# Kernel tuning notes

Measured on AMD Instinct MI355X. Metric: run time of the kernel, lower is better.

Reference implementation:

```python
import jax, jax.numpy as jnp
import numpy as np

N, D, K = 262144, 128, 1024

def setup_inputs() -> dict:
    key = jax.random.key(0)
    kx, km = jax.random.split(key)
    X = jax.random.normal(kx, (N, D), dtype=jnp.float32)
    means = jax.random.normal(km, (K, D), dtype=jnp.float32)
    return {"X": X, "means": means}

def reference(X, means):
    X2 = jnp.sum(X * X, axis=1, keepdims=True)            # [n, 1]
    m2 = jnp.sum(means * means, axis=1)[None, :]          # [1, k]
    dists = X2 - 2.0 * jnp.einsum('nd,kd->nk', X, means) + m2
    assignments = jnp.argmin(dists, axis=1)               # [n]
    approx_X = means[assignments]                         # gather [n, d]
    loss = jnp.sum(jnp.square(X - approx_X))
    return loss
```

## Files before the change

kernel.cpp:

```cpp
#include <hip/hip_runtime.h>
#include <hip/hip_fp8.h>

typedef int v8i __attribute__((ext_vector_type(8)));
typedef float f32x4 __attribute__((ext_vector_type(4)));

#define N_TOTAL 262144
#define D 128
#define K_TOTAL 1024
#define BN 128
#define NBLK (N_TOTAL / BN)
#define TILEB 8192
#define NT 16

__device__ __forceinline__ unsigned umx(unsigned a, unsigned b) {
  return a > b ? a : b;
}

__global__ void prep_means(const float* __restrict__ means,
                           unsigned char* __restrict__ mbf8,
                           float* __restrict__ nm2) {
  int k = blockIdx.x, t = threadIdx.x;
  int ts = k >> 6, c64 = k & 63;
  int cgc = c64 >> 4, c = c64 & 15;
  unsigned char* tb = mbf8 + ts * TILEB + cgc * 2048;
  float v0 = means[k * D + 2 * t];
  float v1 = means[k * D + 2 * t + 1];
  int d0 = 2 * t;
  int kq = d0 >> 5, rem0 = d0 & 31;
  int pk = __builtin_amdgcn_cvt_pk_fp8_f32(v0, v1, 0, false);
  *(unsigned short*)(tb + (kq * 16 + c) * 32 + rem0) = (unsigned short)(pk & 0xFFFF);
  float s = v0 * v0 + v1 * v1;
#pragma unroll
  for (int m = 32; m; m >>= 1) s += __shfl_down(s, m, 64);
  if (t == 0) nm2[k] = -0.5f * s;
}

union BOp {
  uint4 q[2];
  v8i v;
};

__global__ __launch_bounds__(256) void kmeans_main(
    const float* __restrict__ X, const unsigned char* __restrict__ mbf8,
    const float* __restrict__ nm2, float* __restrict__ partials) {
  __shared__ float m2s[K_TOTAL];
  __shared__ float x2s[BN];
  __shared__ float wsum[4];

  const int t = threadIdx.x;
  const int l = t & 63;
  const int w = t >> 6;
  const int lr = l & 15;
  const int kq = l >> 4;
  const long nbase = (long)blockIdx.x * BN;

  v8i af[2];
  float psq[2];
#pragma unroll
  for (int g = 0; g < 2; ++g) {
    const float* xr = X + (nbase + w * 32 + g * 16 + lr) * D + kq * 32;
    v8i av;
    float sq = 0.f;
#pragma unroll
    for (int j = 0; j < 8; ++j) {
      float4 v = *(const float4*)(xr + j * 4);
      sq = fmaf(v.x, v.x, sq);
      sq = fmaf(v.y, v.y, sq);
      sq = fmaf(v.z, v.z, sq);
      sq = fmaf(v.w, v.w, sq);
      int lo = __builtin_amdgcn_cvt_pk_fp8_f32(v.x, v.y, 0, false);
      av[j] = __builtin_amdgcn_cvt_pk_fp8_f32(v.z, v.w, lo, true);
    }
    af[g] = av;
    psq[g] = sq;
  }
#pragma unroll
  for (int g = 0; g < 2; ++g) {
    float s2 = psq[g];
    s2 += __shfl_xor(s2, 16, 64);
    s2 += __shfl_xor(s2, 32, 64);
    if (kq == 0) x2s[w * 32 + g * 16 + lr] = s2;
  }

  {
    float4 v = ((const float4*)nm2)[t];
    *(float4*)(m2s + t * 4) = v;
  }

  float bs[8];
#pragma unroll
  for (int e = 0; e < 8; ++e) bs[e] = -3.402823466e38f;

  __syncthreads();

  const char* bbase = (const char*)mbf8 + l * 32;
  for (int ts = 0; ts < NT; ++ts) {
    const char* tp = bbase + ts * TILEB;
    const float* mp = m2s + ts * 64 + lr;
#pragma unroll
    for (int cgc = 0; cgc < 4; ++cgc) {
      const char* p = tp + cgc * 2048;
      BOp bu;
      bu.q[0] = *(const uint4*)(p);
      bu.q[1] = *(const uint4*)(p + 16);
      float m2v = mp[cgc * 16];
      f32x4 ci = {m2v, m2v, m2v, m2v};
#pragma unroll
      for (int g = 0; g < 2; ++g) {
        f32x4 acc = __builtin_amdgcn_mfma_scale_f32_16x16x128_f8f6f4(
            af[g], bu.v, ci, 0, 0, 0, 127, 0, 127);
#pragma unroll
        for (int e = 0; e < 4; ++e) bs[g * 4 + e] = fmaxf(bs[g * 4 + e], acc[e]);
      }
    }
  }

  float lsum = 0.f;
#pragma unroll
  for (int e = 0; e < 8; ++e) {
    float m = bs[e];
#pragma unroll
    for (int s = 1; s < 16; s <<= 1) {
      float o = __shfl_xor(m, s, 64);
      m = fmaxf(m, o);
    }
    if (lr == 0) {
      int rowc = (e >> 2) * 16 + kq * 4 + (e & 3);
      lsum += x2s[w * 32 + rowc] - 2.0f * m;
    }
  }
#pragma unroll
  for (int s = 32; s; s >>= 1) lsum += __shfl_down(lsum, s, 64);
  if (l == 0) wsum[w] = lsum;
  __syncthreads();
  if (t == 0) partials[blockIdx.x] = wsum[0] + wsum[1] + wsum[2] + wsum[3];
}

__global__ void reduce_loss(const float* __restrict__ partials,
                            float* __restrict__ out) {
  __shared__ double ws[4];
  int t = threadIdx.x;
  double s = 0.0;
  for (int i = t; i < NBLK; i += 256) s += (double)partials[i];
#pragma unroll
  for (int m = 32; m; m >>= 1) s += __shfl_down(s, m, 64);
  if ((t & 63) == 0) ws[t >> 6] = s;
  __syncthreads();
  if (t == 0) out[0] = (float)(ws[0] + ws[1] + ws[2] + ws[3]);
}

extern "C" void kernel_launch(void* const* d_in, const int* in_sizes, int n_in,
                              void* d_out, int out_size, void* d_ws,
                              size_t ws_size, hipStream_t stream) {
  const float* X = (const float*)d_in[0];
  const float* means = (const float*)d_in[1];
  float* out = (float*)d_out;
  char* ws = (char*)d_ws;
  unsigned char* mbf8 = (unsigned char*)ws;
  float* nm2 = (float*)(ws + 131072);
  float* partials = (float*)(ws + 131072 + 4096);

  prep_means<<<K_TOTAL, 64, 0, stream>>>(means, mbf8, nm2);
  kmeans_main<<<NBLK, 256, 0, stream>>>(X, mbf8, nm2, partials);
  reduce_loss<<<1, 256, 0, stream>>>(partials, out);
}
```

Baseline: 74.67 us.

## Split X fp8 conversion into separate prep kernel feeding MFMA-ready layout

Adds a prep_x kernel that converts X to fp8 in the MFMA operand layout and computes row norms into global memory. The main kernel then loads packed fp8 operands directly, with no LDS staging and no __syncthreads before the matmul loop, and reads the centroid norms from global memory. This costs an extra kernel launch plus a write and reread of a 32MB fp8 buffer. A fallback path keeps the old fused kernel when the workspace is too small.

```diff
diff --git a/kernel.cpp b/kernel.cpp
--- a/kernel.cpp
+++ b/kernel.cpp
@@ -12,8 +12,8 @@
 #define TILEB 8192
 #define NT 16
 
-__device__ __forceinline__ unsigned umx(unsigned a, unsigned b) {
-  return a > b ? a : b;
+__device__ __forceinline__ unsigned f2fp8_em(float x) {
+  return (unsigned)__hip_fp8_e4m3(x).__x;
 }
 
 __global__ void prep_means(const float* __restrict__ means,
@@ -28,11 +28,45 @@
   int d0 = 2 * t;
   int kq = d0 >> 5, rem0 = d0 & 31;
   int pk = __builtin_amdgcn_cvt_pk_fp8_f32(v0, v1, 0, false);
-  *(unsigned short*)(tb + (kq * 16 + c) * 32 + rem0) = (unsigned short)(pk & 0xFFFF);
+  *(unsigned short*)(tb + (kq * 16 + c) * 32 + rem0) =
+      (unsigned short)(pk & 0xFFFF);
   float s = v0 * v0 + v1 * v1;
 #pragma unroll
   for (int m = 32; m; m >>= 1) s += __shfl_down(s, m, 64);
   if (t == 0) nm2[k] = -0.5f * s;
+}
+
+__global__ __launch_bounds__(256) void prep_x(const float* __restrict__ X,
+                                              unsigned char* __restrict__ xp,
+                                              float* __restrict__ x2g) {
+  const int t = threadIdx.x;
+  const long row = (long)blockIdx.x * BN + (t >> 1);
+  const int h = t & 1;
+  const float* xr = X + row * D + h * 64;
+  unsigned cw[16];
+  float sq = 0.f;
+#pragma unroll
+  for (int j = 0; j < 16; ++j) {
+    float4 v = *(const float4*)(xr + j * 4);
+    sq = fmaf(v.x, v.x, sq);
+    sq = fmaf(v.y, v.y, sq);
+    sq = fmaf(v.z, v.z, sq);
+    sq = fmaf(v.w, v.w, sq);
+    int lo = __builtin_amdgcn_cvt_pk_fp8_f32(v.x, v.y, 0, false);
+    cw[j] = (unsigned)__builtin_amdgcn_cvt_pk_fp8_f32(v.z, v.w, lo, true);
+  }
+  unsigned char* gb = xp + (row >> 4) * 2048 + (int)(row & 15) * 32;
+#pragma unroll
+  for (int q = 0; q < 2; ++q) {
+    uint4 a, b;
+    a.x = cw[q * 8 + 0]; a.y = cw[q * 8 + 1]; a.z = cw[q * 8 + 2]; a.w = cw[q * 8 + 3];
+    b.x = cw[q * 8 + 4]; b.y = cw[q * 8 + 5]; b.z = cw[q * 8 + 6]; b.w = cw[q * 8 + 7];
+    unsigned char* d0 = gb + (h * 2 + q) * 512;
+    *(uint4*)d0 = a;
+    *(uint4*)(d0 + 16) = b;
+  }
+  float s2 = sq + __shfl_xor(sq, 1, 64);
+  if (h == 0) x2g[row] = s2;
 }
 
 union BOp {
@@ -41,10 +75,9 @@
 };
 
 __global__ __launch_bounds__(256) void kmeans_main(
-    const float* __restrict__ X, const unsigned char* __restrict__ mbf8,
-    const float* __restrict__ nm2, float* __restrict__ partials) {
-  __shared__ float m2s[K_TOTAL];
-  __shared__ float x2s[BN];
+    const unsigned char* __restrict__ xp, const unsigned char* __restrict__ mbf8,
+    const float* __restrict__ nm2, const float* __restrict__ x2g,
+    float* __restrict__ partials) {
   __shared__ float wsum[4];
 
   const int t = threadIdx.x;
@@ -55,6 +88,78 @@
   const long nbase = (long)blockIdx.x * BN;
 
   v8i af[2];
+  {
+    const unsigned char* ap =
+        xp + ((long)blockIdx.x * 8 + w * 2) * 2048 + l * 32;
+    BOp a0, a1;
+    a0.q[0] = *(const uint4*)(ap);
+    a0.q[1] = *(const uint4*)(ap + 16);
+    a1.q[0] = *(const uint4*)(ap + 2048);
+    a1.q[1] = *(const uint4*)(ap + 2048 + 16);
+    af[0] = a0.v;
+    af[1] = a1.v;
+  }
+
+  float bs[8];
+#pragma unroll
+  for (int e = 0; e < 8; ++e) bs[e] = -3.402823466e38f;
+
+  const char* bbase = (const char*)mbf8 + l * 32;
+  const float* mp = nm2 + lr;
+  for (int ts = 0; ts < NT; ++ts) {
+    const char* tp = bbase + ts * TILEB;
+#pragma unroll
+    for (int cgc = 0; cgc < 4; ++cgc) {
+      const char* p = tp + cgc * 2048;
+      BOp bu;
+      bu.q[0] = *(const uint4*)(p);
+      bu.q[1] = *(const uint4*)(p + 16);
+      float m2v = mp[ts * 64 + cgc * 16];
+      f32x4 ci = {m2v, m2v, m2v, m2v};
+#pragma unroll
+      for (int g = 0; g < 2; ++g) {
+        f32x4 acc = __builtin_amdgcn_mfma_scale_f32_16x16x128_f8f6f4(
+            af[g], bu.v, ci, 0, 0, 0, 127, 0, 127);
+#pragma unroll
+        for (int e = 0; e < 4; ++e) bs[g * 4 + e] = fmaxf(bs[g * 4 + e], acc[e]);
+      }
+    }
+  }
+
+  float lsum = 0.f;
+#pragma unroll
+  for (int e = 0; e < 8; ++e) {
+    float m = bs[e];
+#pragma unroll
+    for (int s = 1; s < 16; s <<= 1) {
+      float o = __shfl_xor(m, s, 64);
+      m = fmaxf(m, o);
+    }
+    if (lr == 0) {
+      int rowc = (e >> 2) * 16 + kq * 4 + (e & 3);
+      lsum += x2g[nbase + w * 32 + rowc] - 2.0f * m;
+    }
+  }
+#pragma unroll
+  for (int s = 32; s; s >>= 1) lsum += __shfl_down(lsum, s, 64);
+  if (l == 0) wsum[w] = lsum;
+  __syncthreads();
+  if (t == 0) partials[blockIdx.x] = wsum[0] + wsum[1] + wsum[2] + wsum[3];
+}
+
+__global__ __launch_bounds__(256) void kmeans_main_fb(
+    const float* __restrict__ X, const unsigned char* __restrict__ mbf8,
+    const float* __restrict__ nm2, float* __restrict__ partials) {
+  __shared__ float m2s[K_TOTAL];
+  __shared__ float x2s[BN];
+  __shared__ float wsum[4];
+  const int t = threadIdx.x;
+  const int l = t & 63;
+  const int w = t >> 6;
+  const int lr = l & 15;
+  const int kq = l >> 4;
+  const long nbase = (long)blockIdx.x * BN;
+  v8i af[2];
   float psq[2];
 #pragma unroll
   for (int g = 0; g < 2; ++g) {
@@ -68,8 +173,8 @@
       sq = fmaf(v.y, v.y, sq);
       sq = fmaf(v.z, v.z, sq);
       sq = fmaf(v.w, v.w, sq);
-      int lo = __builtin_amdgcn_cvt_pk_fp8_f32(v.x, v.y, 0, false);
-      av[j] = __builtin_amdgcn_cvt_pk_fp8_f32(v.z, v.w, lo, true);
+      av[j] = (int)(f2fp8_em(v.x) | (f2fp8_em(v.y) << 8) |
+                    (f2fp8_em(v.z) << 16) | (f2fp8_em(v.w) << 24));
     }
     af[g] = av;
     psq[g] = sq;
@@ -81,18 +186,14 @@
     s2 += __shfl_xor(s2, 32, 64);
     if (kq == 0) x2s[w * 32 + g * 16 + lr] = s2;
   }
-
   {
     float4 v = ((const float4*)nm2)[t];
     *(float4*)(m2s + t * 4) = v;
   }
-
   float bs[8];
 #pragma unroll
   for (int e = 0; e < 8; ++e) bs[e] = -3.402823466e38f;
-
-  __syncthreads();
-
+  __syncthreads();
   const char* bbase = (const char*)mbf8 + l * 32;
   for (int ts = 0; ts < NT; ++ts) {
     const char* tp = bbase + ts * TILEB;
@@ -114,7 +215,6 @@
       }
     }
   }
-
   float lsum = 0.f;
 #pragma unroll
   for (int e = 0; e < 8; ++e) {
@@ -159,8 +259,16 @@
   unsigned char* mbf8 = (unsigned char*)ws;
   float* nm2 = (float*)(ws + 131072);
   float* partials = (float*)(ws + 131072 + 4096);
+  float* x2g = (float*)(ws + 131072 + 4096 + 8192);
+  unsigned char* xp = (unsigned char*)(ws + 131072 + 4096 + 8192 + 1048576);
+  const size_t needed = 131072 + 4096 + 8192 + 1048576 + (size_t)N_TOTAL * D;
 
   prep_means<<<K_TOTAL, 64, 0, stream>>>(means, mbf8, nm2);
-  kmeans_main<<<NBLK, 256, 0, stream>>>(X, mbf8, nm2, partials);
+  if (ws_size >= needed) {
+    prep_x<<<NBLK, 256, 0, stream>>>(X, xp, x2g);
+    kmeans_main<<<NBLK, 256, 0, stream>>>(xp, mbf8, nm2, x2g, partials);
+  } else {
+    kmeans_main_fb<<<NBLK, 256, 0, stream>>>(X, mbf8, nm2, partials);
+  }
   reduce_loss<<<1, 256, 0, stream>>>(partials, out);
 }
```

Measured after the change: 89.42 us. 1.2x slower.

## Stage all fp8 means in LDS and process 1024 rows per block

Applied to the files above, without the earlier changes.

Each block now copies the whole 128KB fp8 codebook into shared memory once and has 512 threads each hold 8 row-groups of X fragments, so every B-fragment load is reused across 8 MFMAs instead of 2. The grid shrinks from 2048 to 256 blocks. prep_means now splits each lane's 32-byte fragment into two 16-byte halves so LDS reads are conflict-friendly. In exchange, LDS use rises to about 136KB per block, which may allow only one block per CU. Register pressure also grows (8 A fragments plus 32 max accumulators), and 256 blocks may underfill the 256 CUs with little latency hiding.

```diff
diff --git a/kernel.cpp b/kernel.cpp
--- a/kernel.cpp
+++ b/kernel.cpp
@@ -7,14 +7,9 @@
 #define N_TOTAL 262144
 #define D 128
 #define K_TOTAL 1024
-#define BN 128
-#define NBLK (N_TOTAL / BN)
 #define TILEB 8192
 #define NT 16
-
-__device__ __forceinline__ unsigned umx(unsigned a, unsigned b) {
-  return a > b ? a : b;
-}
+#define NBLK 256
 
 __global__ void prep_means(const float* __restrict__ means,
                            unsigned char* __restrict__ mbf8,
@@ -27,8 +22,10 @@
   float v1 = means[k * D + 2 * t + 1];
   int d0 = 2 * t;
   int kq = d0 >> 5, rem0 = d0 & 31;
+  int l = kq * 16 + c;
+  int off = (rem0 < 16) ? (l * 16 + rem0) : (1024 + l * 16 + (rem0 - 16));
   int pk = __builtin_amdgcn_cvt_pk_fp8_f32(v0, v1, 0, false);
-  *(unsigned short*)(tb + (kq * 16 + c) * 32 + rem0) = (unsigned short)(pk & 0xFFFF);
+  *(unsigned short*)(tb + off) = (unsigned short)(pk & 0xFFFF);
   float s = v0 * v0 + v1 * v1;
 #pragma unroll
   for (int m = 32; m; m >>= 1) s += __shfl_down(s, m, 64);
@@ -40,25 +37,35 @@
   v8i v;
 };
 
-__global__ __launch_bounds__(256) void kmeans_main(
+__global__ __launch_bounds__(512) void kmeans_main(
     const float* __restrict__ X, const unsigned char* __restrict__ mbf8,
     const float* __restrict__ nm2, float* __restrict__ partials) {
+  __shared__ __attribute__((aligned(16))) char cb[NT * TILEB];
   __shared__ float m2s[K_TOTAL];
-  __shared__ float x2s[BN];
-  __shared__ float wsum[4];
+  __shared__ float x2s[1024];
+  __shared__ float wsum[8];
 
   const int t = threadIdx.x;
   const int l = t & 63;
   const int w = t >> 6;
   const int lr = l & 15;
   const int kq = l >> 4;
-  const long nbase = (long)blockIdx.x * BN;
+  const long nbase = (long)blockIdx.x * 1024;
 
-  v8i af[2];
-  float psq[2];
 #pragma unroll
-  for (int g = 0; g < 2; ++g) {
-    const float* xr = X + (nbase + w * 32 + g * 16 + lr) * D + kq * 32;
+  for (int j = 0; j < 16; ++j) {
+    *(uint4*)(cb + j * 8192 + t * 16) =
+        *(const uint4*)((const char*)mbf8 + j * 8192 + t * 16);
+  }
+  if (t < 256) {
+    float4 v = ((const float4*)nm2)[t];
+    *(float4*)(m2s + t * 4) = v;
+  }
+
+  v8i af[8];
+#pragma unroll
+  for (int g = 0; g < 8; ++g) {
+    const float* xr = X + (nbase + w * 128 + g * 16 + lr) * D + kq * 32;
     v8i av;
     float sq = 0.f;
 #pragma unroll
@@ -72,52 +79,41 @@
       av[j] = __builtin_amdgcn_cvt_pk_fp8_f32(v.z, v.w, lo, true);
     }
     af[g] = av;
-    psq[g] = sq;
-  }
-#pragma unroll
-  for (int g = 0; g < 2; ++g) {
-    float s2 = psq[g];
-    s2 += __shfl_xor(s2, 16, 64);
+    float s2 = sq + __shfl_xor(sq, 16, 64);
     s2 += __shfl_xor(s2, 32, 64);
-    if (kq == 0) x2s[w * 32 + g * 16 + lr] = s2;
+    if (kq == 0) x2s[w * 128 + g * 16 + lr] = s2;
   }
 
-  {
-    float4 v = ((const float4*)nm2)[t];
-    *(float4*)(m2s + t * 4) = v;
-  }
-
-  float bs[8];
+  float bs[32];
 #pragma unroll
-  for (int e = 0; e < 8; ++e) bs[e] = -3.402823466e38f;
+  for (int e = 0; e < 32; ++e) bs[e] = -3.402823466e38f;
 
   __syncthreads();
 
-  const char* bbase = (const char*)mbf8 + l * 32;
   for (int ts = 0; ts < NT; ++ts) {
-    const char* tp = bbase + ts * TILEB;
+    const char* tp = cb + ts * TILEB;
     const float* mp = m2s + ts * 64 + lr;
 #pragma unroll
     for (int cgc = 0; cgc < 4; ++cgc) {
-      const char* p = tp + cgc * 2048;
       BOp bu;
-      bu.q[0] = *(const uint4*)(p);
-      bu.q[1] = *(const uint4*)(p + 16);
+      bu.q[0] = *(const uint4*)(tp + cgc * 2048 + l * 16);
+      bu.q[1] = *(const uint4*)(tp + cgc * 2048 + 1024 + l * 16);
       float m2v = mp[cgc * 16];
       f32x4 ci = {m2v, m2v, m2v, m2v};
 #pragma unroll
-      for (int g = 0; g < 2; ++g) {
+      for (int g = 0; g < 8; ++g) {
         f32x4 acc = __builtin_amdgcn_mfma_scale_f32_16x16x128_f8f6f4(
             af[g], bu.v, ci, 0, 0, 0, 127, 0, 127);
 #pragma unroll
-        for (int e = 0; e < 4; ++e) bs[g * 4 + e] = fmaxf(bs[g * 4 + e], acc[e]);
+        for (int e = 0; e < 4; ++e)
+          bs[g * 4 + e] = fmaxf(bs[g * 4 + e], acc[e]);
       }
     }
   }
 
   float lsum = 0.f;
 #pragma unroll
-  for (int e = 0; e < 8; ++e) {
+  for (int e = 0; e < 32; ++e) {
     float m = bs[e];
 #pragma unroll
     for (int s = 1; s < 16; s <<= 1) {
@@ -126,14 +122,19 @@
     }
     if (lr == 0) {
       int rowc = (e >> 2) * 16 + kq * 4 + (e & 3);
-      lsum += x2s[w * 32 + rowc] - 2.0f * m;
+      lsum += x2s[w * 128 + rowc] - 2.0f * m;
     }
   }
 #pragma unroll
   for (int s = 32; s; s >>= 1) lsum += __shfl_down(lsum, s, 64);
   if (l == 0) wsum[w] = lsum;
   __syncthreads();
-  if (t == 0) partials[blockIdx.x] = wsum[0] + wsum[1] + wsum[2] + wsum[3];
+  if (t == 0) {
+    float b = 0.f;
+#pragma unroll
+    for (int j = 0; j < 8; ++j) b += wsum[j];
+    partials[blockIdx.x] = b;
+  }
 }
 
 __global__ void reduce_loss(const float* __restrict__ partials,
@@ -161,6 +162,6 @@
   float* partials = (float*)(ws + 131072 + 4096);
 
   prep_means<<<K_TOTAL, 64, 0, stream>>>(means, mbf8, nm2);
-  kmeans_main<<<NBLK, 256, 0, stream>>>(X, mbf8, nm2, partials);
+  kmeans_main<<<NBLK, 512, 0, stream>>>(X, mbf8, nm2, partials);
   reduce_loss<<<1, 256, 0, stream>>>(partials, out);
 }
```

After: 61.64 us. 17.4% less time.
